# Kernel tuning notes

Hardware: AMD Instinct MI355X
Metric: run time of the kernel (lower is better)

## Reference

```python
import jax, jax.numpy as jnp
import numpy as np

B, S, HID = 1, 2048, 2048
N_HEADS = 16
HEAD_DIM = HID // N_HEADS  # 128
ROPE_THETA = 10000.0
NEG_INF = -1e9


def setup_inputs() -> dict:
    key = jax.random.key(0)
    ks = jax.random.split(key, 5)
    hidden_states = jax.random.normal(ks[0], (B, S, HID), dtype=jnp.float32)
    scale = 1.0 / np.sqrt(HID)
    Wq = jax.random.normal(ks[1], (HID, HID), dtype=jnp.float32) * scale
    Wk = jax.random.normal(ks[2], (HID, HID), dtype=jnp.float32) * scale
    Wv = jax.random.normal(ks[3], (HID, HID), dtype=jnp.float32) * scale
    Wo = jax.random.normal(ks[4], (HID, HID), dtype=jnp.float32) * scale
    # additive causal mask [B, 1, S, S]: 0 on/below diag, -1e9 above
    causal = jnp.tril(jnp.ones((S, S), dtype=bool))
    attention_mask = jnp.where(causal, 0.0, NEG_INF).astype(jnp.float32)[None, None]
    attention_mask = jnp.broadcast_to(attention_mask, (B, 1, S, S))
    position_ids = jnp.broadcast_to(jnp.arange(S, dtype=jnp.int64)[None, :], (B, S))
    return {"hidden_states": hidden_states, "Wq": Wq, "Wk": Wk, "Wv": Wv,
            "Wo": Wo, "attention_mask": attention_mask, "position_ids": position_ids}


def _rotate_half(x):
    x1, x2 = jnp.split(x, 2, axis=-1)
    return jnp.concatenate((-x2, x1), axis=-1)


def _rope_cos_sin(position_ids, head_dim, dtype):
    inv_freq = 1.0 / (ROPE_THETA ** (jnp.arange(0, head_dim, 2, dtype=jnp.float32) / head_dim))
    freqs = position_ids.astype(jnp.float32)[:, :, None] * inv_freq[None, None, :]  # [b, s, d/2]
    emb = jnp.concatenate((freqs, freqs), axis=-1)  # [b, s, d]
    # unsqueeze_dim=1 -> broadcast over heads
    return jnp.cos(emb).astype(dtype)[:, None], jnp.sin(emb).astype(dtype)[:, None]


def reference(hidden_states, Wq, Wk, Wv, Wo, attention_mask, position_ids):
    b, s, h = hidden_states.shape
    d = HEAD_DIM
    def proj(W):
        return (hidden_states @ W.T).reshape(b, s, N_HEADS, d).transpose(0, 2, 1, 3)  # [b,h,s,d]
    q, k, v = proj(Wq), proj(Wk), proj(Wv)
    cos, sin = _rope_cos_sin(position_ids, d, q.dtype)
    q = q * cos + _rotate_half(q) * sin
    k = k * cos + _rotate_half(k) * sin
    scores = jnp.einsum('bhqd,bhkd->bhqk', q, k) / jnp.sqrt(jnp.float32(d))
    scores = scores + attention_mask
    probs = jax.nn.softmax(scores.astype(jnp.float32), axis=-1).astype(q.dtype)
    attn = jnp.einsum('bhqk,bhkd->bhqd', probs, v)
    out = attn.transpose(0, 2, 1, 3).reshape(b, s, h)
    return out @ Wo.T
```

## Files before the change

kernel.cpp:

```cpp
#include <hip/hip_runtime.h>

typedef _Float16 half8 __attribute__((ext_vector_type(8)));
typedef _Float16 half4 __attribute__((ext_vector_type(4)));
typedef float floatx4 __attribute__((ext_vector_type(4)));
typedef float floatx16 __attribute__((ext_vector_type(16)));

#define GLDS(gp, lp) __builtin_amdgcn_global_load_lds( \
    (const __attribute__((address_space(1))) void*)(gp), \
    (__attribute__((address_space(3))) void*)(lp), 16, 0, 0)

__global__ void cvt_f2h5(const float* __restrict__ s0, const float* __restrict__ s1,
                         const float* __restrict__ s2, const float* __restrict__ s3,
                         const float* __restrict__ s4,
                         _Float16* __restrict__ d0, _Float16* __restrict__ d1,
                         _Float16* __restrict__ d2, _Float16* __restrict__ d3,
                         _Float16* __restrict__ d4, int n8) {
  int i = blockIdx.x * 256 + threadIdx.x;
  if (i >= n8) return;
  const float* s; _Float16* d;
  switch (blockIdx.y) {
    case 0: s = s0; d = d0; break;
    case 1: s = s1; d = d1; break;
    case 2: s = s2; d = d2; break;
    case 3: s = s3; d = d3; break;
    default: s = s4; d = d4; break;
  }
  const float4* s4p = (const float4*)s;
  float4 a = s4p[2 * i], b = s4p[2 * i + 1];
  half8 h;
  h[0] = (_Float16)a.x; h[1] = (_Float16)a.y; h[2] = (_Float16)a.z; h[3] = (_Float16)a.w;
  h[4] = (_Float16)b.x; h[5] = (_Float16)b.y; h[6] = (_Float16)b.z; h[7] = (_Float16)b.w;
  *(half8*)(d + 8 * (size_t)i) = h;
}

__global__ __launch_bounds__(256) void transpose_k(const _Float16* __restrict__ src,
                                                   _Float16* __restrict__ dst) {
  __shared__ _Float16 t[64][72];
  const int r0 = blockIdx.y * 64, c0 = blockIdx.x * 64;
  const int tr = threadIdx.x >> 3, tc = (threadIdx.x & 7) * 8;
  #pragma unroll
  for (int p = 0; p < 2; ++p) {
    half8 v = *(const half8*)(src + (size_t)(r0 + p * 32 + tr) * 2048 + c0 + tc);
    *(half8*)&t[p * 32 + tr][tc] = v;
  }
  __syncthreads();
  #pragma unroll
  for (int p = 0; p < 2; ++p) {
    half8 v;
    #pragma unroll
    for (int j = 0; j < 8; ++j) v[j] = t[tc + j][p * 32 + tr];
    *(half8*)(dst + (size_t)(c0 + p * 32 + tr) * 2048 + r0 + tc) = v;
  }
}

template <int OUTF, int BN>
__global__ __launch_bounds__(256) void gemm_nt(const _Float16* __restrict__ A,
                                               const _Float16* __restrict__ B,
                                               _Float16* __restrict__ Ch,
                                               float* __restrict__ Cf,
                                               long long bStride, long long cStride) {
  __shared__ _Float16 As[2][128 * 32];
  __shared__ _Float16 Bs[2][BN * 32];
  const int NF = BN / 32;
  const int tid = threadIdx.x, lane = tid & 63, wv = tid >> 6;
  const int fr = lane & 15, fg = lane >> 4;
  const int bm = blockIdx.y * 128, bn = blockIdx.x * BN;
  const _Float16* Ab = A + (size_t)bm * 2048;
  const _Float16* Bb = B + (size_t)blockIdx.z * bStride + (size_t)bn * 2048;
  const int srow = lane >> 2;
  const int gsw = (lane & 3) ^ ((lane >> 3) & 3);
  const int asw = (fr >> 1) & 3;

  floatx4 acc[4][NF] = {};

  auto stage = [&](int buf, int kt) {
    #pragma unroll
    for (int r = 0; r < 2; ++r) {
      int row = r * 64 + wv * 16 + srow;
      GLDS(Ab + (size_t)row * 2048 + kt * 32 + gsw * 8, &As[buf][(r * 64 + wv * 16) * 32]);
    }
    #pragma unroll
    for (int r = 0; r < BN / 64; ++r) {
      int row = r * 64 + wv * 16 + srow;
      GLDS(Bb + (size_t)row * 2048 + kt * 32 + gsw * 8, &Bs[buf][(r * 64 + wv * 16) * 32]);
    }
  };
  const int wm = (wv >> 1) * 64, wn = (wv & 1) * (BN / 2);

  stage(0, 0);
  __syncthreads();

  #pragma unroll 2
  for (int kt = 0; kt < 64; ++kt) {
    const int cur = kt & 1;
    if (kt < 63) stage(cur ^ 1, kt + 1);
    half8 af[4], bf[NF];
    #pragma unroll
    for (int m = 0; m < 4; ++m)
      af[m] = *(const half8*)&As[cur][(wm + m * 16 + fr) * 32 + ((fg ^ asw) * 8)];
    #pragma unroll
    for (int n = 0; n < NF; ++n)
      bf[n] = *(const half8*)&Bs[cur][(wn + n * 16 + fr) * 32 + ((fg ^ asw) * 8)];
    #pragma unroll
    for (int m = 0; m < 4; ++m)
      #pragma unroll
      for (int n = 0; n < NF; ++n)
        acc[m][n] = __builtin_amdgcn_mfma_f32_16x16x32_f16(af[m], bf[n], acc[m][n], 0, 0, 0);
    __syncthreads();
  }

  #pragma unroll
  for (int m = 0; m < 4; ++m)
    #pragma unroll
    for (int n = 0; n < NF; ++n)
      #pragma unroll
      for (int i = 0; i < 4; ++i) {
        const int row = bm + wm + m * 16 + fg * 4 + i;
        const int col = bn + wn + n * 16 + fr;
        if (OUTF)
          Cf[(size_t)row * 2048 + col] = acc[m][n][i];
        else
          Ch[(size_t)blockIdx.z * cStride + (size_t)row * 2048 + col] = (_Float16)acc[m][n][i];
      }
}

__global__ void rope_k(_Float16* __restrict__ Q, _Float16* __restrict__ K) {
  const int idx = blockIdx.x * 256 + threadIdx.x;
  const int s = idx >> 10;
  const int hd = idx & 1023;
  const int head = hd >> 6, d = hd & 63;
  const float freq = powf(10000.0f, -(float)d * (1.0f / 64.0f));
  const float ang = (float)s * freq;
  float sn, c;
  sincosf(ang, &sn, &c);
  const size_t base = (size_t)s * 2048 + head * 128 + d;
  float q1 = (float)Q[base], q2 = (float)Q[base + 64];
  Q[base]      = (_Float16)(q1 * c - q2 * sn);
  Q[base + 64] = (_Float16)(q2 * c + q1 * sn);
  float k1 = (float)K[base], k2 = (float)K[base + 64];
  K[base]      = (_Float16)(k1 * c - k2 * sn);
  K[base + 64] = (_Float16)(k2 * c + k1 * sn);
}

__global__ __launch_bounds__(256, 2) void attn_k(const _Float16* __restrict__ Qp,
                                                 const _Float16* __restrict__ Kp,
                                                 const _Float16* __restrict__ Vt,
                                                 _Float16* __restrict__ Po,
                                                 float* __restrict__ Pr) {
  extern __shared__ _Float16 smem[];
  _Float16* Ks = smem;
  _Float16* Vs = smem + 2 * 64 * 128;
  _Float16* Pb = smem + 4 * 64 * 128;

  const int tid = threadIdx.x, lane = tid & 63, wv = tid >> 6;
  const int l31 = lane & 31, hi = lane >> 5;
  const int wq = wv >> 1, wk = wv & 1;

  const int bid = (int)blockIdx.x;
  const int head = ((bid & 7) << 1) | ((bid >> 3) & 1);
  const int L = bid >> 4;
  int g, it0, itEnd;
  if (L < 16) { g = 16 + L; it0 = 0; itEnd = 16; }
  else {
    const int j = (L - 16) >> 1;
    if ((L & 1) == 0) { g = 15 - j; it0 = 0; itEnd = g + 1; }
    else             { g = 31 - j; it0 = 16; itEnd = g + 1; }
  }
  const size_t hoff = (size_t)head * 128;
  const int qw = g * 64 + wq * 32;
  _Float16* Pw = Pb + wv * (32 * 40);

  half8 qf[8];
  const _Float16 scl = (_Float16)0.08838834764831845f;
  #pragma unroll
  for (int ks = 0; ks < 8; ++ks) {
    half8 t = *(const half8*)(Qp + (size_t)(qw + l31) * 2048 + hoff + ks * 16 + hi * 8);
    #pragma unroll
    for (int j = 0; j < 8; ++j) t[j] = (_Float16)(t[j] * scl);
    qf[ks] = t;
  }

  auto stage = [&](int buf, int it) {
    const int kv0 = it * 64;
    #pragma unroll
    for (int i = 0; i < 4; ++i) {
      const int rbase = wv * 16 + i * 4;
      const int row = rbase + (lane >> 4);
      const int gr = (lane & 15) ^ (row & 7);
      GLDS(Kp + (size_t)(kv0 + row) * 2048 + hoff + gr * 8,
           Ks + buf * 8192 + rbase * 128);
    }
    #pragma unroll
    for (int i = 0; i < 4; ++i) {
      const int rbase = wv * 32 + i * 8;
      const int row = rbase + (lane >> 3);
      const int gr = (lane & 7) ^ (row & 7);
      GLDS(Vt + (size_t)(hoff + row) * 2048 + kv0 + gr * 8,
           Vs + buf * 8192 + rbase * 64);
    }
  };

  floatx16 o[4] = {};
  float rsum = 0.0f;

  stage(0, it0);
  __syncthreads();

  int buf = 0;
  for (int it = it0; it < itEnd; ++it) {
    if (it + 1 < itEnd) stage(buf ^ 1, it + 1);
    const _Float16* Kb = Ks + buf * 8192;
    const _Float16* Vb = Vs + buf * 8192;

    const int krow = wk * 32 + l31;
    const int ksw = l31 & 7;
    floatx16 S = {};
    __builtin_amdgcn_s_setprio(1);
    #pragma unroll
    for (int ks = 0; ks < 8; ++ks) {
      half8 a = *(const half8*)(Kb + krow * 128 + (((ks * 2 + hi) ^ ksw) * 8));
      S = __builtin_amdgcn_mfma_f32_32x32x16_f16(a, qf[ks], S, 0, 0, 0);
    }
    __builtin_amdgcn_s_setprio(0);

    if (it == g) {
      const int kv0 = it * 64;
      const int qa = qw + l31;
      #pragma unroll
      for (int r = 0; r < 16; ++r) {
        const int ka = kv0 + wk * 32 + (r & 3) + 8 * (r >> 2) + 4 * hi;
        if (ka > qa) S[r] = -1e30f;
      }
    }

    #pragma unroll
    for (int r4 = 0; r4 < 4; ++r4) {
      float p0 = __expf(S[4 * r4 + 0] - 8.0f);
      float p1 = __expf(S[4 * r4 + 1] - 8.0f);
      float p2 = __expf(S[4 * r4 + 2] - 8.0f);
      float p3 = __expf(S[4 * r4 + 3] - 8.0f);
      rsum += (p0 + p1) + (p2 + p3);
      half4 pk;
      pk[0] = (_Float16)p0; pk[1] = (_Float16)p1;
      pk[2] = (_Float16)p2; pk[3] = (_Float16)p3;
      *(half4*)(Pw + l31 * 40 + r4 * 8 + hi * 4) = pk;
    }

    half8 pa0 = *(const half8*)(Pw + l31 * 40 + hi * 8);
    half8 pa1 = *(const half8*)(Pw + l31 * 40 + 16 + hi * 8);

    __builtin_amdgcn_s_setprio(1);
    #pragma unroll
    for (int dt = 0; dt < 4; ++dt) {
      const int vrow = dt * 32 + l31;
      const int vsw = vrow & 7;
      half8 b0 = *(const half8*)(Vb + vrow * 64 + (((wk * 4 + hi) ^ vsw) * 8));
      half8 b1 = *(const half8*)(Vb + vrow * 64 + (((wk * 4 + 2 + hi) ^ vsw) * 8));
      o[dt] = __builtin_amdgcn_mfma_f32_32x32x16_f16(pa0, b0, o[dt], 0, 0, 0);
      o[dt] = __builtin_amdgcn_mfma_f32_32x32x16_f16(pa1, b1, o[dt], 0, 0, 0);
    }
    __builtin_amdgcn_s_setprio(0);

    __syncthreads();
    buf ^= 1;
  }

  float* Mo = (float*)smem;
  float* Mr = (float*)(smem + 16384);
  if (wk == 1) {
    #pragma unroll
    for (int dt = 0; dt < 4; ++dt)
      #pragma unroll
      for (int r = 0; r < 16; ++r)
        Mo[((wq * 4 + dt) * 16 + r) * 64 + lane] = o[dt][r];
    Mr[wq * 64 + lane] = rsum;
  }
  __syncthreads();
  if (wk == 0) {
    rsum += Mr[wq * 64 + lane];
    float rs = rsum;
    rs += __shfl_xor(rs, 32);
    if (hi == 0) Pr[(size_t)bid * 64 + wq * 32 + l31] = rs;
    #pragma unroll
    for (int dt = 0; dt < 4; ++dt)
      #pragma unroll
      for (int r = 0; r < 16; ++r) {
        const float w = o[dt][r] + Mo[((wq * 4 + dt) * 16 + r) * 64 + lane];
        const int ql = wq * 32 + (r & 3) + 8 * (r >> 2) + 4 * hi;
        Po[(size_t)bid * 8192 + ql * 128 + dt * 32 + l31] = (_Float16)w;
      }
  }
}

__global__ __launch_bounds__(256) void attn_merge(const _Float16* __restrict__ Po,
                                                  const float* __restrict__ Pr,
                                                  _Float16* __restrict__ At) {
  const int bidx = (int)blockIdx.x;
  const int h = bidx & 15, g = bidx >> 4;
  const int hb = ((h & 1) << 3) | (h >> 1);
  const int L0 = (g >= 16) ? (g - 16) : (16 + 2 * (15 - g));
  const int U0 = L0 * 16 + hb;
  const bool two = (g >= 16);
  const int U1 = two ? ((17 + 2 * (31 - g)) * 16 + hb) : 0;
  const int t = threadIdx.x;
  const int q = t >> 2, cs = t & 3;
  const float r0 = Pr[(size_t)U0 * 64 + q];
  const float r1 = two ? Pr[(size_t)U1 * 64 + q] : 0.0f;
  const float inv = 1.0f / (r0 + r1);
  const size_t orow = (size_t)(g * 64 + q) * 2048 + h * 128;
  #pragma unroll
  for (int s = 0; s < 4; ++s) {
    const int d0 = (cs + s * 4) * 8;
    half8 a = *(const half8*)(Po + (size_t)U0 * 8192 + q * 128 + d0);
    half8 o;
    if (two) {
      half8 b = *(const half8*)(Po + (size_t)U1 * 8192 + q * 128 + d0);
      #pragma unroll
      for (int j = 0; j < 8; ++j) o[j] = (_Float16)(((float)a[j] + (float)b[j]) * inv);
    } else {
      #pragma unroll
      for (int j = 0; j < 8; ++j) o[j] = (_Float16)((float)a[j] * inv);
    }
    *(half8*)(At + orow + d0) = o;
  }
}

extern "C" void kernel_launch(void* const* d_in, const int* in_sizes, int n_in,
                              void* d_out, int out_size, void* d_ws, size_t ws_size,
                              hipStream_t stream) {
  (void)in_sizes; (void)n_in; (void)out_size; (void)ws_size;
  const float* X  = (const float*)d_in[0];
  const float* Wq = (const float*)d_in[1];
  const float* Wk = (const float*)d_in[2];
  const float* Wv = (const float*)d_in[3];
  const float* Wo = (const float*)d_in[4];
  float* out = (float*)d_out;

  const size_t SZ = 2048ull * 2048ull;
  _Float16* ws  = (_Float16*)d_ws;
  _Float16* Xh  = ws + 0 * SZ;
  _Float16* Wqh = ws + 1 * SZ;
  _Float16* Wkh = ws + 2 * SZ;
  _Float16* Wvh = ws + 3 * SZ;
  _Float16* Woh = ws + 4 * SZ;
  _Float16* Qp  = ws + 5 * SZ;
  _Float16* Kp  = ws + 6 * SZ;
  _Float16* Vp  = ws + 7 * SZ;
  _Float16* Vtg = Wqh;
  _Float16* At  = Xh;
  _Float16* Po  = Wkh;
  float*    Pr  = (float*)Vp;

  const int n8 = (int)(SZ / 8);
  dim3 blk(256);

  cvt_f2h5<<<dim3(n8 / 256, 5), blk, 0, stream>>>(X, Wq, Wk, Wv, Wo,
                                                  Xh, Wqh, Wkh, Wvh, Woh, n8);

  gemm_nt<0, 128><<<dim3(16, 16, 3), blk, 0, stream>>>(Xh, Wqh, Qp, nullptr,
                                                       (long long)SZ, (long long)SZ);
  rope_k<<<(2048 * 1024) / 256, blk, 0, stream>>>(Qp, Kp);
  transpose_k<<<dim3(32, 32), blk, 0, stream>>>(Vp, Vtg);

  const size_t attn_lds = (4 * 64 * 128 + 4 * 32 * 40) * sizeof(_Float16);
  attn_k<<<768, blk, attn_lds, stream>>>(Qp, Kp, Vtg, Po, Pr);
  attn_merge<<<512, blk, 0, stream>>>(Po, Pr, At);

  gemm_nt<1, 64><<<dim3(32, 16, 1), blk, 0, stream>>>(At, Woh, nullptr, out, 0, 0);
}
```

Measured before the change: 179.9 us.

## Use 256x256-tile 8-wave GEMM with 4-stage LDS pipeline for QKV projection

Replaces the 128x128-tile, 256-thread QKV projection GEMM with a new 512-thread kernel that computes 256x256 output tiles. It uses a 4-deep global_load_lds ring buffer (128KB of LDS) with explicit vmcnt waits, and splits each K-step into two MFMA halves with setprio raised during compute. The aim is more operand reuse per tile and better overlap of loads with MFMA work. In exchange it launches only 192 blocks, which may underfill the CUs, and the epilogue writes output element by element without vectorization.

Measured after the change: 174.9 us. -2.8%, faster.

```diff
diff --git a/kernel.cpp b/kernel.cpp
--- a/kernel.cpp
+++ b/kernel.cpp
@@ -51,6 +51,112 @@
     for (int j = 0; j < 8; ++j) v[j] = t[tc + j][p * 32 + tr];
     *(half8*)(dst + (size_t)(c0 + p * 32 + tr) * 2048 + r0 + tc) = v;
   }
+}
+
+template <int OUTF>
+__global__ __launch_bounds__(512, 2) void gemm8(const _Float16* __restrict__ A,
+                                                const _Float16* __restrict__ B,
+                                                _Float16* __restrict__ Ch,
+                                                float* __restrict__ Cf,
+                                                long long bStride, long long cStride) {
+  extern __shared__ _Float16 lds[];
+  _Float16* As = lds;
+  _Float16* Bs = lds + 4 * 8192;
+
+  const int tid = threadIdx.x, lane = tid & 63, wv = tid >> 6;
+  const int fr = lane & 15, fg = lane >> 4;
+  const int wm = wv >> 2, wn = wv & 3;
+  const int bm = blockIdx.y * 256, bn = blockIdx.x * 256;
+  const _Float16* Ab = A + (size_t)bm * 2048;
+  const _Float16* Bb = B + (size_t)blockIdx.z * bStride + (size_t)bn * 2048;
+
+  const int srow = lane >> 2;
+  const int gsw = (lane & 3) ^ ((srow >> 1) & 3);
+  const int asw = (fr >> 1) & 3;
+
+  auto stageA = [&](int t) {
+    const int kc = t * 32;
+    _Float16* dst = As + (t & 3) * 8192;
+    #pragma unroll
+    for (int g = 0; g < 2; ++g) {
+      const int rb = wv * 32 + g * 16;
+      GLDS(Ab + (size_t)(rb + srow) * 2048 + kc + gsw * 8, dst + rb * 32);
+    }
+  };
+  auto stageB = [&](int t) {
+    const int kc = t * 32;
+    _Float16* dst = Bs + (t & 3) * 8192;
+    #pragma unroll
+    for (int g = 0; g < 2; ++g) {
+      const int rb = wv * 32 + g * 16;
+      GLDS(Bb + (size_t)(rb + srow) * 2048 + kc + gsw * 8, dst + rb * 32);
+    }
+  };
+
+  floatx4 acc[8][4] = {};
+
+  stageA(0); stageB(0);
+  stageA(1); stageB(1);
+  stageA(2); stageB(2);
+
+  for (int t = 0; t < 64; ++t) {
+    const _Float16* Ac = As + (t & 3) * 8192;
+    const _Float16* Bc = Bs + (t & 3) * 8192;
+    if (t + 3 < 64) stageA(t + 3);
+    const int rem = 63 - t;
+    if (rem >= 3)      asm volatile("s_waitcnt vmcnt(10)" ::: "memory");
+    else if (rem == 2) asm volatile("s_waitcnt vmcnt(8)" ::: "memory");
+    else if (rem == 1) asm volatile("s_waitcnt vmcnt(4)" ::: "memory");
+    else               asm volatile("s_waitcnt vmcnt(0)" ::: "memory");
+    __builtin_amdgcn_s_barrier();
+
+    half8 bf[4], af[4];
+    #pragma unroll
+    for (int n = 0; n < 4; ++n)
+      bf[n] = *(const half8*)(Bc + (wn * 64 + n * 16 + fr) * 32 + ((fg ^ asw) * 8));
+    #pragma unroll
+    for (int m = 0; m < 4; ++m)
+      af[m] = *(const half8*)(Ac + (wm * 128 + m * 16 + fr) * 32 + ((fg ^ asw) * 8));
+    asm volatile("s_waitcnt lgkmcnt(0)" ::: "memory");
+    __builtin_amdgcn_sched_barrier(0);
+    __builtin_amdgcn_s_setprio(1);
+    #pragma unroll
+    for (int m = 0; m < 4; ++m)
+      #pragma unroll
+      for (int n = 0; n < 4; ++n)
+        acc[m][n] = __builtin_amdgcn_mfma_f32_16x16x32_f16(af[m], bf[n], acc[m][n], 0, 0, 0);
+    __builtin_amdgcn_s_setprio(0);
+    __builtin_amdgcn_s_barrier();
+
+    if (t + 3 < 64) stageB(t + 3);
+    #pragma unroll
+    for (int m = 0; m < 4; ++m)
+      af[m] = *(const half8*)(Ac + (wm * 128 + 64 + m * 16 + fr) * 32 + ((fg ^ asw) * 8));
+    asm volatile("s_waitcnt lgkmcnt(0)" ::: "memory");
+    __builtin_amdgcn_sched_barrier(0);
+    __builtin_amdgcn_s_setprio(1);
+    #pragma unroll
+    for (int m = 0; m < 4; ++m)
+      #pragma unroll
+      for (int n = 0; n < 4; ++n)
+        acc[m + 4][n] = __builtin_amdgcn_mfma_f32_16x16x32_f16(af[m], bf[n], acc[m + 4][n], 0, 0, 0);
+    __builtin_amdgcn_s_setprio(0);
+    __builtin_amdgcn_s_barrier();
+  }
+
+  #pragma unroll
+  for (int m = 0; m < 8; ++m)
+    #pragma unroll
+    for (int n = 0; n < 4; ++n)
+      #pragma unroll
+      for (int i = 0; i < 4; ++i) {
+        const int row = bm + wm * 128 + m * 16 + fg * 4 + i;
+        const int col = bn + wn * 64 + n * 16 + fr;
+        if (OUTF)
+          Cf[(size_t)row * 2048 + col] = acc[m][n][i];
+        else
+          Ch[(size_t)blockIdx.z * cStride + (size_t)row * 2048 + col] = (_Float16)acc[m][n][i];
+      }
 }
 
 template <int OUTF, int BN>
@@ -357,8 +463,8 @@
   cvt_f2h5<<<dim3(n8 / 256, 5), blk, 0, stream>>>(X, Wq, Wk, Wv, Wo,
                                                   Xh, Wqh, Wkh, Wvh, Woh, n8);
 
-  gemm_nt<0, 128><<<dim3(16, 16, 3), blk, 0, stream>>>(Xh, Wqh, Qp, nullptr,
-                                                       (long long)SZ, (long long)SZ);
+  gemm8<0><<<dim3(8, 8, 3), dim3(512), 131072, stream>>>(Xh, Wqh, Qp, nullptr,
+                                                         (long long)SZ, (long long)SZ);
   rope_k<<<(2048 * 1024) / 256, blk, 0, stream>>>(Qp, Kp);
   transpose_k<<<dim3(32, 32), blk, 0, stream>>>(Vp, Vtg);
 
```

## Add fused 256x192 QKV GEMM with triple-buffered LDS pipeline and faster RoPE

Applied to the files above, without the earlier changes.

Replaces the batched three-way QKV projection with a single 512-thread GEMM over the concatenated weights (Wq, Wk, Wv contiguous). It uses 256x192 tiles, a 64-wide K step, three LDS stages for A and two for B filled by global_load_lds, and MFMA priority boosting. The aim is more data reuse per tile and better overlap of loads with compute. RoPE now uses exp2f and __sincosf in place of powf and sincosf, and the output GEMM switches to 128-wide N tiles. Costs: one workgroup per CU because of the 144KB LDS, and fast sincos loses accuracy at large angles.

Result: faster. 168.7 us (-6.3%).

```diff
diff --git a/kernel.cpp b/kernel.cpp
--- a/kernel.cpp
+++ b/kernel.cpp
@@ -51,6 +51,100 @@
     for (int j = 0; j < 8; ++j) v[j] = t[tc + j][p * 32 + tr];
     *(half8*)(dst + (size_t)(c0 + p * 32 + tr) * 2048 + r0 + tc) = v;
   }
+}
+
+__global__ __launch_bounds__(512, 1) void gemm_qkv(const _Float16* __restrict__ A,
+                                                   const _Float16* __restrict__ W,
+                                                   _Float16* __restrict__ Cq) {
+  extern __shared__ _Float16 lds[];
+  _Float16* As = lds;
+  _Float16* Bs = lds + 3 * 16384;
+
+  const int tid = threadIdx.x, lane = tid & 63, wv = tid >> 6;
+  const int fr = lane & 15, fg = lane >> 4;
+  const int wm = wv >> 2, wn = wv & 3;
+  const int bm = blockIdx.y * 256, bn = blockIdx.x * 192;
+  const _Float16* Ab = A + (size_t)bm * 2048;
+  const _Float16* Bb = W + (size_t)bn * 2048;
+
+  const int srow = lane >> 3;
+  const int sgr = (lane & 7) ^ srow;
+
+  auto stageA = [&](int t) {
+    _Float16* dst = As + (t % 3) * 16384;
+    const size_t coff = (size_t)t * 64 + sgr * 8;
+    #pragma unroll
+    for (int i = 0; i < 4; ++i) {
+      const int rb = wv * 32 + i * 8;
+      GLDS(Ab + (size_t)(rb + srow) * 2048 + coff, dst + rb * 64);
+    }
+  };
+  auto stageB = [&](int t) {
+    _Float16* dst = Bs + (t & 1) * 12288;
+    const size_t coff = (size_t)t * 64 + sgr * 8;
+    #pragma unroll
+    for (int i = 0; i < 3; ++i) {
+      const int rb = wv * 24 + i * 8;
+      GLDS(Bb + (size_t)(rb + srow) * 2048 + coff, dst + rb * 64);
+    }
+  };
+
+  const int arow = wm * 128 + fr;
+  const int brow = wn * 48 + fr;
+  const int sw = fr & 7;
+
+  floatx4 acc[8][3] = {};
+
+  stageA(0); stageB(0); stageA(1);
+  asm volatile("s_waitcnt vmcnt(4)" ::: "memory");
+  __builtin_amdgcn_s_barrier();
+
+  for (int t = 0; t < 32; ++t) {
+    const _Float16* Ac = As + (t % 3) * 16384;
+    const _Float16* Bc = Bs + (t & 1) * 12288;
+    #pragma unroll
+    for (int p = 0; p < 4; ++p) {
+      const int kh = p >> 1, qm = p & 1;
+      const int sl = ((kh * 4 + fg) ^ sw) * 8;
+      half8 af[4], bf[3];
+      #pragma unroll
+      for (int m = 0; m < 4; ++m)
+        af[m] = *(const half8*)(Ac + (arow + qm * 64 + m * 16) * 64 + sl);
+      #pragma unroll
+      for (int n = 0; n < 3; ++n)
+        bf[n] = *(const half8*)(Bc + (brow + n * 16) * 64 + sl);
+      if (p == 0 && t + 1 < 32) stageB(t + 1);
+      if (p == 2 && t + 2 < 32) stageA(t + 2);
+      __builtin_amdgcn_s_barrier();
+      asm volatile("s_waitcnt lgkmcnt(0)" ::: "memory");
+      __builtin_amdgcn_sched_barrier(0);
+      __builtin_amdgcn_s_setprio(1);
+      #pragma unroll
+      for (int m = 0; m < 4; ++m)
+        #pragma unroll
+        for (int n = 0; n < 3; ++n)
+          acc[qm * 4 + m][n] =
+              __builtin_amdgcn_mfma_f32_16x16x32_f16(af[m], bf[n], acc[qm * 4 + m][n], 0, 0, 0);
+      __builtin_amdgcn_s_setprio(0);
+      if (p == 3) {
+        if (t < 30)       asm volatile("s_waitcnt vmcnt(4)" ::: "memory");
+        else if (t == 30) asm volatile("s_waitcnt vmcnt(0)" ::: "memory");
+      }
+      __builtin_amdgcn_s_barrier();
+    }
+  }
+
+  #pragma unroll
+  for (int m = 0; m < 8; ++m)
+    #pragma unroll
+    for (int n = 0; n < 3; ++n)
+      #pragma unroll
+      for (int i = 0; i < 4; ++i) {
+        const int row = bm + wm * 128 + m * 16 + fg * 4 + i;
+        const int col = bn + wn * 48 + n * 16 + fr;
+        Cq[(size_t)(col >> 11) * 4194304 + (size_t)row * 2048 + (col & 2047)] =
+            (_Float16)acc[m][n][i];
+      }
 }
 
 template <int OUTF, int BN>
@@ -129,10 +223,10 @@
   const int s = idx >> 10;
   const int hd = idx & 1023;
   const int head = hd >> 6, d = hd & 63;
-  const float freq = powf(10000.0f, -(float)d * (1.0f / 64.0f));
+  const float freq = exp2f((float)d * -0.2076205059304601f);
   const float ang = (float)s * freq;
   float sn, c;
-  sincosf(ang, &sn, &c);
+  __sincosf(ang, &sn, &c);
   const size_t base = (size_t)s * 2048 + head * 128 + d;
   float q1 = (float)Q[base], q2 = (float)Q[base + 64];
   Q[base]      = (_Float16)(q1 * c - q2 * sn);
@@ -357,8 +451,7 @@
   cvt_f2h5<<<dim3(n8 / 256, 5), blk, 0, stream>>>(X, Wq, Wk, Wv, Wo,
                                                   Xh, Wqh, Wkh, Wvh, Woh, n8);
 
-  gemm_nt<0, 128><<<dim3(16, 16, 3), blk, 0, stream>>>(Xh, Wqh, Qp, nullptr,
-                                                       (long long)SZ, (long long)SZ);
+  gemm_qkv<<<dim3(32, 8), dim3(512), 147456, stream>>>(Xh, Wqh, Qp);
   rope_k<<<(2048 * 1024) / 256, blk, 0, stream>>>(Qp, Kp);
   transpose_k<<<dim3(32, 32), blk, 0, stream>>>(Vp, Vtg);
 
@@ -366,5 +459,5 @@
   attn_k<<<768, blk, attn_lds, stream>>>(Qp, Kp, Vtg, Po, Pr);
   attn_merge<<<512, blk, 0, stream>>>(Po, Pr, At);
 
-  gemm_nt<1, 64><<<dim3(32, 16, 1), blk, 0, stream>>>(At, Woh, nullptr, out, 0, 0);
-}
+  gemm_nt<1, 128><<<dim3(16, 16, 1), blk, 0, stream>>>(At, Woh, nullptr, out, 0, 0);
+}
```

## Add dedicated 128x192 triple-buffered QKV GEMM and retune output GEMM tile

Applied to the files above, without the earlier changes.

Replaces the batched QKV GEMM with a fused kernel that treats Wq/Wk/Wv as one 6144-row weight matrix and uses 128x192 tiles. It runs a three-stage global_load_lds pipeline with explicit waitcnt, barriers and setprio around the MFMA block, aiming for better operand reuse and load/compute overlap. RoPE switches to exp2f and the fast __sincosf intrinsic, which may cost accuracy at large angles. The output projection GEMM moves from BN=64 to BN=128, halving the grid.

Result: faster. 174.1 us (-3.2%).

```diff
diff --git a/kernel.cpp b/kernel.cpp
--- a/kernel.cpp
+++ b/kernel.cpp
@@ -51,6 +51,88 @@
     for (int j = 0; j < 8; ++j) v[j] = t[tc + j][p * 32 + tr];
     *(half8*)(dst + (size_t)(c0 + p * 32 + tr) * 2048 + r0 + tc) = v;
   }
+}
+
+__global__ __launch_bounds__(256, 2) void gemm_qkv(const _Float16* __restrict__ A,
+                                                   const _Float16* __restrict__ W,
+                                                   _Float16* __restrict__ Cq) {
+  extern __shared__ _Float16 lds[];
+  _Float16* As = lds;
+  _Float16* Bs = lds + 3 * 4096;
+
+  const int tid = threadIdx.x, lane = tid & 63, wv = tid >> 6;
+  const int fr = lane & 15, fg = lane >> 4;
+  const int wm = wv >> 1, wn = wv & 1;
+  const int bm = blockIdx.y * 128, bn = blockIdx.x * 192;
+  const _Float16* Ab = A + (size_t)bm * 2048;
+  const _Float16* Bb = W + (size_t)bn * 2048;
+
+  const int srow = lane >> 2;
+  const int gsw = (lane & 3) ^ ((lane >> 3) & 3);
+  const int asw = (fr >> 1) & 3;
+
+  auto stageA = [&](int t) {
+    _Float16* dst = As + (t % 3) * 4096;
+    const size_t coff = (size_t)t * 32 + gsw * 8;
+    #pragma unroll
+    for (int r = 0; r < 2; ++r) {
+      const int rb = wv * 32 + r * 16;
+      GLDS(Ab + (size_t)(rb + srow) * 2048 + coff, dst + rb * 32);
+    }
+  };
+  auto stageB = [&](int t) {
+    _Float16* dst = Bs + (t % 3) * 6144;
+    const size_t coff = (size_t)t * 32 + gsw * 8;
+    #pragma unroll
+    for (int r = 0; r < 3; ++r) {
+      const int rb = wv * 48 + r * 16;
+      GLDS(Bb + (size_t)(rb + srow) * 2048 + coff, dst + rb * 32);
+    }
+  };
+
+  floatx4 acc[4][6] = {};
+
+  stageA(0); stageB(0);
+  stageA(1); stageB(1);
+  asm volatile("s_waitcnt vmcnt(5)" ::: "memory");
+  __builtin_amdgcn_s_barrier();
+
+  for (int t = 0; t < 64; ++t) {
+    const _Float16* Ac = As + (t % 3) * 4096;
+    const _Float16* Bc = Bs + (t % 3) * 6144;
+    half8 af[4], bf[6];
+    #pragma unroll
+    for (int m = 0; m < 4; ++m)
+      af[m] = *(const half8*)(Ac + (wm * 64 + m * 16 + fr) * 32 + ((fg ^ asw) * 8));
+    #pragma unroll
+    for (int n = 0; n < 6; ++n)
+      bf[n] = *(const half8*)(Bc + (wn * 96 + n * 16 + fr) * 32 + ((fg ^ asw) * 8));
+    if (t + 2 < 64) { stageA(t + 2); stageB(t + 2); }
+    asm volatile("s_waitcnt lgkmcnt(0)" ::: "memory");
+    __builtin_amdgcn_sched_barrier(0);
+    __builtin_amdgcn_s_setprio(1);
+    #pragma unroll
+    for (int m = 0; m < 4; ++m)
+      #pragma unroll
+      for (int n = 0; n < 6; ++n)
+        acc[m][n] = __builtin_amdgcn_mfma_f32_16x16x32_f16(af[m], bf[n], acc[m][n], 0, 0, 0);
+    __builtin_amdgcn_s_setprio(0);
+    if (t < 62) asm volatile("s_waitcnt vmcnt(5)" ::: "memory");
+    else        asm volatile("s_waitcnt vmcnt(0)" ::: "memory");
+    __builtin_amdgcn_s_barrier();
+  }
+
+  #pragma unroll
+  for (int m = 0; m < 4; ++m)
+    #pragma unroll
+    for (int n = 0; n < 6; ++n)
+      #pragma unroll
+      for (int i = 0; i < 4; ++i) {
+        const int row = bm + wm * 64 + m * 16 + fg * 4 + i;
+        const int col = bn + wn * 96 + n * 16 + fr;
+        Cq[(size_t)(col >> 11) * 4194304 + (size_t)row * 2048 + (col & 2047)] =
+            (_Float16)acc[m][n][i];
+      }
 }
 
 template <int OUTF, int BN>
@@ -129,10 +211,10 @@
   const int s = idx >> 10;
   const int hd = idx & 1023;
   const int head = hd >> 6, d = hd & 63;
-  const float freq = powf(10000.0f, -(float)d * (1.0f / 64.0f));
+  const float freq = exp2f((float)d * -0.2076205059304601f);
   const float ang = (float)s * freq;
   float sn, c;
-  sincosf(ang, &sn, &c);
+  __sincosf(ang, &sn, &c);
   const size_t base = (size_t)s * 2048 + head * 128 + d;
   float q1 = (float)Q[base], q2 = (float)Q[base + 64];
   Q[base]      = (_Float16)(q1 * c - q2 * sn);
@@ -357,8 +439,7 @@
   cvt_f2h5<<<dim3(n8 / 256, 5), blk, 0, stream>>>(X, Wq, Wk, Wv, Wo,
                                                   Xh, Wqh, Wkh, Wvh, Woh, n8);
 
-  gemm_nt<0, 128><<<dim3(16, 16, 3), blk, 0, stream>>>(Xh, Wqh, Qp, nullptr,
-                                                       (long long)SZ, (long long)SZ);
+  gemm_qkv<<<dim3(32, 16), dim3(256), 61440, stream>>>(Xh, Wqh, Qp);
   rope_k<<<(2048 * 1024) / 256, blk, 0, stream>>>(Qp, Kp);
   transpose_k<<<dim3(32, 32), blk, 0, stream>>>(Vp, Vtg);
 
@@ -366,5 +447,5 @@
   attn_k<<<768, blk, attn_lds, stream>>>(Qp, Kp, Vtg, Po, Pr);
   attn_merge<<<512, blk, 0, stream>>>(Po, Pr, At);
 
-  gemm_nt<1, 64><<<dim3(32, 16, 1), blk, 0, stream>>>(At, Woh, nullptr, out, 0, 0);
-}
+  gemm_nt<1, 128><<<dim3(16, 16, 1), blk, 0, stream>>>(At, Woh, nullptr, out, 0, 0);
+}
```
